# Optimization experiments

Measured on AMD Instinct MI355X. Metric: run time of the kernel, lower is better.

The kernel has to match this reference:

```python
import jax, jax.numpy as jnp
import numpy as np

B, N, D_IN = 8, 8192, 13
RATIO, R, K = 0.25, 0.2, 32


def setup_inputs() -> dict:
    key = jax.random.key(0)
    k1, k2, k3, k4 = jax.random.split(key, 4)
    x = jax.random.normal(k1, (B, N, D_IN), dtype=jnp.float32)
    pos = jax.random.uniform(k2, (B, N, 3), dtype=jnp.float32)
    batch = jnp.broadcast_to(jnp.arange(B, dtype=jnp.int32)[:, None], (B, N))
    W1 = jax.random.normal(k3, (D_IN + 3, 64), dtype=jnp.float32) * 0.1
    b1 = jnp.zeros((64,), jnp.float32)
    W2 = jax.random.normal(k4, (64, 128), dtype=jnp.float32) * 0.1
    b2 = jnp.zeros((128,), jnp.float32)
    return {"x": x, "pos": pos, "batch": batch, "W1": W1, "b1": b1, "W2": W2, "b2": b2}


def _fps_single(p, M):
    """Deterministic farthest point sampling (start at index 0). p: [N,3] -> [M] int32."""
    n = p.shape[0]

    def step(carry, _):
        mind, last = carry
        d = jnp.sum((p - p[last]) ** 2, axis=-1)
        mind = jnp.minimum(mind, d)
        nxt = jnp.argmax(mind).astype(jnp.int32)
        return (mind, nxt), nxt

    init = (jnp.full((n,), 1e10, p.dtype), jnp.int32(0))
    _, rest = jax.lax.scan(step, init, None, length=M - 1)
    return jnp.concatenate([jnp.zeros((1,), jnp.int32), rest])


def reference(x, pos, batch, W1, b1, W2, b2):
    M = int(RATIO * N)
    # --- FPS per cloud ---
    idx = jax.vmap(lambda p: _fps_single(p, M))(pos)              # [B, M]
    pos_s = jnp.take_along_axis(pos, idx[..., None], axis=1)      # [B, M, 3]
    # --- radius ball query: first K in-ball neighbors by point index ---
    d2 = jnp.sum((pos_s[:, :, None, :] - pos[:, None, :, :]) ** 2, axis=-1)  # [B, M, N]
    within = d2 <= R * R
    rank = jnp.where(within, jnp.arange(N, dtype=jnp.int32), N)   # invalid -> N
    negv, nbr = jax.lax.top_k(-rank, K)                           # K smallest ranks
    valid = negv > -N                                             # [B, M, K]
    # --- gather -> local_nn MLP -> masked max-scatter (PointNetConv) ---
    x_j = jax.vmap(lambda a, i: a[i])(x, nbr)                     # [B, M, K, D_IN]
    pos_j = jax.vmap(lambda a, i: a[i])(pos, nbr)                 # [B, M, K, 3]
    feat = jnp.concatenate([x_j, pos_j - pos_s[:, :, None, :]], axis=-1)
    h = jax.nn.relu(feat @ W1 + b1)
    h = jax.nn.relu(h @ W2 + b2)                                  # [B, M, K, 128]
    h = jnp.where(valid[..., None], h, -jnp.inf)
    x_out = jnp.max(h, axis=2)                                    # [B, M, 128]
    batch_s = jnp.take_along_axis(batch, idx, axis=1)             # [B, M]
    return x_out, pos_s, batch_s
```

## Files before the change

kernel.cpp:

```cpp
#include <hip/hip_runtime.h>
#include <cstddef>

#define B_   8
#define N_   8192
#define M_   2048
#define K_   32
#define DIN_ 13

typedef _Float16 f16x8 __attribute__((ext_vector_type(8)));
typedef float    f32x4 __attribute__((ext_vector_type(4)));

template <int CTRL>
__device__ __forceinline__ float dppmax(float v) {
  int o = __builtin_amdgcn_update_dpp(
      (int)0xff800000, __float_as_int(v), CTRL, 0xF, 0xF, false);
  return fmaxf(v, __int_as_float(o));
}
template <int CTRL>
__device__ __forceinline__ float dppminf(float v) {
  int o = __builtin_amdgcn_update_dpp(
      (int)0x7f800000, __float_as_int(v), CTRL, 0xF, 0xF, false);
  return fminf(v, __int_as_float(o));
}
template <int CTRL>
__device__ __forceinline__ unsigned dppminu(unsigned v) {
  unsigned o = (unsigned)__builtin_amdgcn_update_dpp(
      (int)0xFFFFFFFF, (int)v, CTRL, 0xF, 0xF, false);
  return v < o ? v : o;
}
__device__ __forceinline__ float wave_reduce_max(float v) {
  v = dppmax<0x111>(v); v = dppmax<0x112>(v); v = dppmax<0x114>(v);
  v = dppmax<0x118>(v); v = dppmax<0x142>(v); v = dppmax<0x143>(v);
  return __int_as_float(__builtin_amdgcn_readlane(__float_as_int(v), 63));
}
__device__ __forceinline__ unsigned wave_reduce_min_u32(unsigned v) {
  v = dppminu<0x111>(v); v = dppminu<0x112>(v); v = dppminu<0x114>(v);
  v = dppminu<0x118>(v); v = dppminu<0x142>(v); v = dppminu<0x143>(v);
  return (unsigned)__builtin_amdgcn_readlane((int)v, 63);
}

__global__ __launch_bounds__(1024, 4) void fps_kernel(
    const float* __restrict__ pos,
    float* __restrict__ pos_s,
    float* __restrict__ batch_s)
{
  const int b    = blockIdx.x;
  const int t    = threadIdx.x;
  const int lane = t & 63;
  const int wid  = t >> 6;
  const float* p = pos + (size_t)b * N_ * 3;

  __shared__ float px_l[N_], py_l[N_], pz_l[N_];
  __shared__ int   r2o[N_];
  __shared__ int   vbase[512];
  __shared__ int   vcur[512];
  __shared__ int   wsum[8];
  __shared__ unsigned long long kslot[3];

  for (int mm = t; mm < M_; mm += 1024)
    batch_s[b * M_ + mm] = (float)b;
  if (t < 512) vcur[t] = 0;
  if (t == 0) { kslot[0] = 0ull; kslot[1] = 0ull; kslot[2] = 0ull; }
  __syncthreads();

  int vid[8];
#pragma unroll
  for (int i = 0; i < 8; ++i) {
    int j = t + 1024 * i;
    float x = p[j * 3 + 0], y = p[j * 3 + 1], z = p[j * 3 + 2];
    px_l[j] = x; py_l[j] = y; pz_l[j] = z;
    int ix = (int)(x * 8.f); ix = ix < 0 ? 0 : (ix > 7 ? 7 : ix);
    int iy = (int)(y * 8.f); iy = iy < 0 ? 0 : (iy > 7 ? 7 : iy);
    int iz = (int)(z * 8.f); iz = iz < 0 ? 0 : (iz > 7 ? 7 : iz);
    int v = (ix & 1) | ((iy & 1) << 1) | ((iz & 1) << 2) |
            (((ix >> 1) & 1) << 3) | (((iy >> 1) & 1) << 4) |
            (((iz >> 1) & 1) << 5) |
            ((ix >> 2) << 6) | ((iy >> 2) << 7) | ((iz >> 2) << 8);
    vid[i] = v;
    atomicAdd(&vcur[v], 1);
  }
  __syncthreads();

  int h = 0, sc = 0;
  if (t < 512) {
    h = vcur[t]; sc = h;
#pragma unroll
    for (int d = 1; d < 64; d <<= 1) {
      int o = __shfl_up(sc, d);
      if (lane >= d) sc += o;
    }
    if (lane == 63) wsum[wid] = sc;
  }
  __syncthreads();
  if (t < 8) {
    int v = wsum[t]; int inc = v;
#pragma unroll
    for (int d = 1; d < 8; d <<= 1) {
      int o = __shfl_up(inc, d);
      if (t >= d) inc += o;
    }
    wsum[t] = inc - v;
  }
  __syncthreads();
  if (t < 512) { vbase[t] = sc - h + wsum[t >> 6]; vcur[t] = 0; }
  __syncthreads();

#pragma unroll
  for (int i = 0; i < 8; ++i) {
    int j = t + 1024 * i;
    int r = vbase[vid[i]] + atomicAdd(&vcur[vid[i]], 1);
    r2o[r] = j;
  }
  __syncthreads();

  float px[8], py[8], pz[8], mind[8]; int oi[8];
#pragma unroll
  for (int i = 0; i < 8; ++i) {
    int o = r2o[t * 8 + i];
    oi[i] = o;
    px[i] = px_l[o]; py[i] = py_l[o]; pz[i] = pz_l[o];
    mind[i] = 1e10f;
  }
#pragma unroll
  for (int i = 0; i < 8; ++i) {
    asm volatile("" : "+v"(px[i]), "+v"(py[i]), "+v"(pz[i]));
  }

  float bxmin = px[0], bxmax = px[0], bymin = py[0], bymax = py[0],
        bzmin = pz[0], bzmax = pz[0];
#pragma unroll
  for (int i = 1; i < 8; ++i) {
    bxmin = fminf(bxmin, px[i]); bxmax = fmaxf(bxmax, px[i]);
    bymin = fminf(bymin, py[i]); bymax = fmaxf(bymax, py[i]);
    bzmin = fminf(bzmin, pz[i]); bzmax = fmaxf(bzmax, pz[i]);
  }

  float lx = px_l[0], ly = py_l[0], lz = pz_l[0];
  if (t == 0) {
    pos_s[(size_t)b * M_ * 3 + 0] = lx;
    pos_s[(size_t)b * M_ * 3 + 1] = ly;
    pos_s[(size_t)b * M_ * 3 + 2] = lz;
  }

  float ltm = 1e10f;
  float cwm = 0.f;
  unsigned cmin = 0xFFFFFFFFu;
  int sl = 1;
  int rs = 0;

  for (int s = 1; s < M_; ++s) {
    float cx = fmaxf(fmaxf(bxmin - lx, lx - bxmax), 0.f);
    float cy = fmaxf(fmaxf(bymin - ly, ly - bymax), 0.f);
    float cz = fmaxf(fmaxf(bzmin - lz, lz - bzmax), 0.f);
    float LB = (cx * cx + cy * cy) + cz * cz;
    bool lp = (LB * 0.999999f < ltm);
    if (__ballot(lp) != 0ull) {
      float tmax;
      {
#pragma clang fp contract(off)
#pragma unroll
        for (int i = 0; i < 8; ++i) {
          float dx = px[i] - lx, dy = py[i] - ly, dz = pz[i] - lz;
          float d  = (dx * dx + dy * dy) + dz * dz;
          mind[i]  = fminf(mind[i], d);
        }
        float m0 = fmaxf(mind[0], mind[1]), m1 = fmaxf(mind[2], mind[3]);
        float m2 = fmaxf(mind[4], mind[5]), m3 = fmaxf(mind[6], mind[7]);
        tmax = fmaxf(fmaxf(m0, m1), fmaxf(m2, m3));
      }
      ltm = tmax;
      const float wm = wave_reduce_max(tmax);
      cwm = wm;
      unsigned cc = 0xFFFFFFFFu;
#pragma unroll
      for (int i = 0; i < 8; ++i) {
        unsigned cand = (mind[i] == wm) ? (unsigned)oi[i] : 0xFFFFFFFFu;
        cc = cc < cand ? cc : cand;
      }
      cmin = wave_reduce_min_u32(cc);
    }
    if (lane == 0) {
      unsigned long long key =
          ((unsigned long long)__float_as_uint(cwm) << 32) |
          (unsigned long long)(0xFFFFFFFFu - cmin);
      atomicMax(&kslot[sl], key);
    }
    __syncthreads();
    if (t == 0) kslot[rs] = 0ull;
    const unsigned long long kk = kslot[sl];
    const int wj  = (int)(0xFFFFFFFFu - (unsigned int)(kk & 0xFFFFFFFFull));
    const int wju = (int)__builtin_amdgcn_readfirstlane(wj);
    lx = px_l[wju]; ly = py_l[wju]; lz = pz_l[wju];
    if (t == 0) {
      size_t o2 = ((size_t)b * M_ + s) * 3;
      pos_s[o2 + 0] = lx; pos_s[o2 + 1] = ly; pos_s[o2 + 2] = lz;
    }
    sl = (sl == 2) ? 0 : sl + 1;
    rs = (rs == 2) ? 0 : rs + 1;
  }
}

__global__ __launch_bounds__(256) void prep_kernel(
    const float* __restrict__ W1, const float* __restrict__ W2,
    _Float16* __restrict__ w1t, _Float16* __restrict__ w2t)
{
  int t = blockIdx.x * 256 + threadIdx.x;
  if (t < 8192) {
    int n = t >> 6, k = t & 63;
    w2t[t] = (_Float16)W2[k * 128 + n];
  }
  int u = t - 8192;
  if (u >= 0 && u < 1024) {
    int n = u >> 4, k = u & 15;
    w1t[u] = (_Float16)W1[k * 64 + n];
  }
}

__global__ __launch_bounds__(64) void sa_kernel(
    const float* __restrict__ x,
    const float* __restrict__ pos,
    const float* __restrict__ b1,
    const float* __restrict__ b2,
    const float* __restrict__ pos_s,
    const _Float16* __restrict__ w1t,
    const _Float16* __restrict__ w2t,
    float* __restrict__ x_out)
{
  const int blk  = blockIdx.x;
  const int b    = blk >> 11;
  const int m    = blk & 2047;
  const int lane = threadIdx.x;
  const int l15  = lane & 15;
  const int quad = lane >> 4;

  __shared__ int      nbr[K_];
  __shared__ _Float16 featb[K_][24];
  __shared__ _Float16 h1b[K_][72];

  const float* pb = pos + (size_t)b * N_ * 3;
  const float* xb = x   + (size_t)b * N_ * DIN_;
  const size_t so = ((size_t)b * M_ + m) * 3;
  const float sx = pos_s[so + 0];
  const float sy = pos_s[so + 1];
  const float sz = pos_s[so + 2];
  const float R2 = (float)(0.2 * 0.2);

  int cnt = 0;
  for (int base = 0; base < N_ && cnt < K_; base += 64) {
    int j = base + lane;
    float qx = pb[j * 3 + 0], qy = pb[j * 3 + 1], qz = pb[j * 3 + 2];
    bool win;
    {
#pragma clang fp contract(off)
      float dx = sx - qx, dy = sy - qy, dz = sz - qz;
      float d2 = (dx * dx + dy * dy) + dz * dz;
      win = d2 <= R2;
    }
    unsigned long long mk = __ballot(win);
    int rank = (int)__popcll(mk & ((1ull << lane) - 1ull));
    if (win) {
      int slot = cnt + rank;
      if (slot < K_) nbr[slot] = j;
    }
    cnt += (int)__popcll(mk);
  }
  const int valid = cnt < K_ ? cnt : K_;
  __syncthreads();

  for (int tq = lane; tq < K_ * 16; tq += 64) {
    int r = tq >> 4, i = tq & 15;
    float v = 0.f;
    if (r < valid) {
      int j = nbr[r];
      if (i < DIN_) {
        v = xb[j * DIN_ + i];
      } else {
        float c = (i == 13) ? sx : (i == 14) ? sy : sz;
        float q = pb[j * 3 + (i - 13)];
        v = q - c;
      }
    }
    featb[r][i] = (_Float16)v;
  }
  __syncthreads();

  f16x8 fz;
#pragma unroll
  for (int i = 0; i < 8; ++i) fz[i] = (_Float16)0;

  f16x8 a1[2], b1f[4];
#pragma unroll
  for (int mt = 0; mt < 2; ++mt)
    a1[mt] = (quad < 2) ? *(const f16x8*)&featb[mt * 16 + l15][quad * 8] : fz;
#pragma unroll
  for (int nt = 0; nt < 4; ++nt)
    b1f[nt] = (quad < 2) ? *(const f16x8*)&w1t[(nt * 16 + l15) * 16 + quad * 8]
                         : fz;

#pragma unroll
  for (int mt = 0; mt < 2; ++mt) {
#pragma unroll
    for (int nt = 0; nt < 4; ++nt) {
      f32x4 c = {0.f, 0.f, 0.f, 0.f};
      c = __builtin_amdgcn_mfma_f32_16x16x32_f16(a1[mt], b1f[nt], c, 0, 0, 0);
      float bb = b1[nt * 16 + l15];
#pragma unroll
      for (int r = 0; r < 4; ++r) {
        float v = c[r] + bb;
        h1b[mt * 16 + quad * 4 + r][nt * 16 + l15] =
            (_Float16)(v > 0.f ? v : 0.f);
      }
    }
  }
  __syncthreads();

  f16x8 a2[2][2];
#pragma unroll
  for (int mt = 0; mt < 2; ++mt)
#pragma unroll
    for (int kt = 0; kt < 2; ++kt)
      a2[mt][kt] = *(const f16x8*)&h1b[mt * 16 + l15][kt * 32 + quad * 8];

  float* o = x_out + ((size_t)b * M_ + m) * 128;
#pragma unroll
  for (int nt = 0; nt < 8; ++nt) {
    f16x8 b20 = *(const f16x8*)&w2t[(nt * 16 + l15) * 64 + 0 * 32 + quad * 8];
    f16x8 b21 = *(const f16x8*)&w2t[(nt * 16 + l15) * 64 + 1 * 32 + quad * 8];
    f32x4 c0 = {0.f, 0.f, 0.f, 0.f}, c1 = {0.f, 0.f, 0.f, 0.f};
    c0 = __builtin_amdgcn_mfma_f32_16x16x32_f16(a2[0][0], b20, c0, 0, 0, 0);
    c0 = __builtin_amdgcn_mfma_f32_16x16x32_f16(a2[0][1], b21, c0, 0, 0, 0);
    c1 = __builtin_amdgcn_mfma_f32_16x16x32_f16(a2[1][0], b20, c1, 0, 0, 0);
    c1 = __builtin_amdgcn_mfma_f32_16x16x32_f16(a2[1][1], b21, c1, 0, 0, 0);
    float bv = b2[nt * 16 + l15];
    float acc = -INFINITY;
#pragma unroll
    for (int r = 0; r < 4; ++r) {
      int row0 = quad * 4 + r;
      int row1 = 16 + quad * 4 + r;
      float v0 = c0[r] + bv; v0 = v0 > 0.f ? v0 : 0.f;
      float v1 = c1[r] + bv; v1 = v1 > 0.f ? v1 : 0.f;
      if (row0 < valid) acc = fmaxf(acc, v0);
      if (row1 < valid) acc = fmaxf(acc, v1);
    }
    acc = fmaxf(acc, __shfl_xor(acc, 16));
    acc = fmaxf(acc, __shfl_xor(acc, 32));
    if (quad == 0) o[nt * 16 + l15] = acc;
  }
}

extern "C" void kernel_launch(void* const* d_in, const int* in_sizes, int n_in,
                              void* d_out, int out_size, void* d_ws, size_t ws_size,
                              hipStream_t stream) {
  (void)in_sizes; (void)n_in; (void)ws_size; (void)out_size;
  const float* x   = (const float*)d_in[0];
  const float* pos = (const float*)d_in[1];
  const float* W1  = (const float*)d_in[3];
  const float* b1  = (const float*)d_in[4];
  const float* W2  = (const float*)d_in[5];
  const float* b2  = (const float*)d_in[6];

  float* out     = (float*)d_out;
  float* x_out   = out;
  float* pos_s   = out + (size_t)B_ * M_ * 128;
  float* batch_s = pos_s + (size_t)B_ * M_ * 3;

  _Float16* w1t = (_Float16*)d_ws;
  _Float16* w2t = w1t + 1024;

  prep_kernel<<<36, 256, 0, stream>>>(W1, W2, w1t, w2t);
  fps_kernel<<<B_, 1024, 0, stream>>>(pos, pos_s, batch_s);
  sa_kernel<<<B_ * M_, 64, 0, stream>>>(x, pos, b1, b2, pos_s, w1t, w2t, x_out);
}
```

Baseline: 1.503 ms.

## Halve FPS block size and replace shared atomicMax with per-wave key DPP reduction

The farthest-point-sampling kernel now runs 512 threads per cloud, each holding 16 points instead of 8. Each step, every wave writes its packed (distance, index) key to a double-buffered shared slot instead of doing a shared 64-bit atomicMax. After the barrier, each wave reduces the 8 wave keys with a DPP max and reads the winner, which removes the triple-slot rotation and its reset. The aim is a cheaper per-step barrier and no atomic contention on the sequential critical path, at the cost of more distance work per thread and more register pressure.

```diff
diff --git a/kernel.cpp b/kernel.cpp
--- a/kernel.cpp
+++ b/kernel.cpp
@@ -17,12 +17,6 @@
   return fmaxf(v, __int_as_float(o));
 }
 template <int CTRL>
-__device__ __forceinline__ float dppminf(float v) {
-  int o = __builtin_amdgcn_update_dpp(
-      (int)0x7f800000, __float_as_int(v), CTRL, 0xF, 0xF, false);
-  return fminf(v, __int_as_float(o));
-}
-template <int CTRL>
 __device__ __forceinline__ unsigned dppminu(unsigned v) {
   unsigned o = (unsigned)__builtin_amdgcn_update_dpp(
       (int)0xFFFFFFFF, (int)v, CTRL, 0xF, 0xF, false);
@@ -38,8 +32,18 @@
   v = dppminu<0x118>(v); v = dppminu<0x142>(v); v = dppminu<0x143>(v);
   return (unsigned)__builtin_amdgcn_readlane((int)v, 63);
 }
-
-__global__ __launch_bounds__(1024, 4) void fps_kernel(
+template <int CTRL>
+__device__ __forceinline__ void dppmax_u64(unsigned &hi, unsigned &lo) {
+  unsigned ohi = (unsigned)__builtin_amdgcn_update_dpp(
+      0, (int)hi, CTRL, 0xF, 0xF, false);
+  unsigned olo = (unsigned)__builtin_amdgcn_update_dpp(
+      0, (int)lo, CTRL, 0xF, 0xF, false);
+  bool g = (ohi > hi) || (ohi == hi && olo > lo);
+  hi = g ? ohi : hi;
+  lo = g ? olo : lo;
+}
+
+__global__ __launch_bounds__(512) void fps_kernel(
     const float* __restrict__ pos,
     float* __restrict__ pos_s,
     float* __restrict__ batch_s)
@@ -55,18 +59,17 @@
   __shared__ int   vbase[512];
   __shared__ int   vcur[512];
   __shared__ int   wsum[8];
-  __shared__ unsigned long long kslot[3];
-
-  for (int mm = t; mm < M_; mm += 1024)
+  __shared__ unsigned long long wkey[2][8];
+
+  for (int mm = t; mm < M_; mm += 512)
     batch_s[b * M_ + mm] = (float)b;
-  if (t < 512) vcur[t] = 0;
-  if (t == 0) { kslot[0] = 0ull; kslot[1] = 0ull; kslot[2] = 0ull; }
-  __syncthreads();
-
-  int vid[8];
-#pragma unroll
-  for (int i = 0; i < 8; ++i) {
-    int j = t + 1024 * i;
+  vcur[t] = 0;
+  __syncthreads();
+
+  int vid[16];
+#pragma unroll
+  for (int i = 0; i < 16; ++i) {
+    int j = t + 512 * i;
     float x = p[j * 3 + 0], y = p[j * 3 + 1], z = p[j * 3 + 2];
     px_l[j] = x; py_l[j] = y; pz_l[j] = z;
     int ix = (int)(x * 8.f); ix = ix < 0 ? 0 : (ix > 7 ? 7 : ix);
@@ -81,16 +84,13 @@
   }
   __syncthreads();
 
-  int h = 0, sc = 0;
-  if (t < 512) {
-    h = vcur[t]; sc = h;
-#pragma unroll
-    for (int d = 1; d < 64; d <<= 1) {
-      int o = __shfl_up(sc, d);
-      if (lane >= d) sc += o;
-    }
-    if (lane == 63) wsum[wid] = sc;
-  }
+  int h = vcur[t], sc = h;
+#pragma unroll
+  for (int d = 1; d < 64; d <<= 1) {
+    int o = __shfl_up(sc, d);
+    if (lane >= d) sc += o;
+  }
+  if (lane == 63) wsum[wid] = sc;
   __syncthreads();
   if (t < 8) {
     int v = wsum[t]; int inc = v;
@@ -102,34 +102,35 @@
     wsum[t] = inc - v;
   }
   __syncthreads();
-  if (t < 512) { vbase[t] = sc - h + wsum[t >> 6]; vcur[t] = 0; }
-  __syncthreads();
-
-#pragma unroll
-  for (int i = 0; i < 8; ++i) {
-    int j = t + 1024 * i;
+  vbase[t] = sc - h + wsum[t >> 6];
+  vcur[t]  = 0;
+  __syncthreads();
+
+#pragma unroll
+  for (int i = 0; i < 16; ++i) {
+    int j = t + 512 * i;
     int r = vbase[vid[i]] + atomicAdd(&vcur[vid[i]], 1);
     r2o[r] = j;
   }
   __syncthreads();
 
-  float px[8], py[8], pz[8], mind[8]; int oi[8];
-#pragma unroll
-  for (int i = 0; i < 8; ++i) {
-    int o = r2o[t * 8 + i];
+  float px[16], py[16], pz[16], mind[16]; int oi[16];
+#pragma unroll
+  for (int i = 0; i < 16; ++i) {
+    int o = r2o[t * 16 + i];
     oi[i] = o;
     px[i] = px_l[o]; py[i] = py_l[o]; pz[i] = pz_l[o];
     mind[i] = 1e10f;
   }
 #pragma unroll
-  for (int i = 0; i < 8; ++i) {
+  for (int i = 0; i < 16; ++i) {
     asm volatile("" : "+v"(px[i]), "+v"(py[i]), "+v"(pz[i]));
   }
 
   float bxmin = px[0], bxmax = px[0], bymin = py[0], bymax = py[0],
         bzmin = pz[0], bzmax = pz[0];
 #pragma unroll
-  for (int i = 1; i < 8; ++i) {
+  for (int i = 1; i < 16; ++i) {
     bxmin = fminf(bxmin, px[i]); bxmax = fmaxf(bxmax, px[i]);
     bymin = fminf(bymin, py[i]); bymax = fmaxf(bymax, py[i]);
     bzmin = fminf(bzmin, pz[i]); bzmax = fmaxf(bzmax, pz[i]);
@@ -143,10 +144,7 @@
   }
 
   float ltm = 1e10f;
-  float cwm = 0.f;
-  unsigned cmin = 0xFFFFFFFFu;
-  int sl = 1;
-  int rs = 0;
+  unsigned long long ckey = 0;
 
   for (int s = 1; s < M_; ++s) {
     float cx = fmaxf(fmaxf(bxmin - lx, lx - bxmax), 0.f);
@@ -159,44 +157,43 @@
       {
 #pragma clang fp contract(off)
 #pragma unroll
-        for (int i = 0; i < 8; ++i) {
+        for (int i = 0; i < 16; ++i) {
           float dx = px[i] - lx, dy = py[i] - ly, dz = pz[i] - lz;
           float d  = (dx * dx + dy * dy) + dz * dz;
           mind[i]  = fminf(mind[i], d);
         }
-        float m0 = fmaxf(mind[0], mind[1]), m1 = fmaxf(mind[2], mind[3]);
-        float m2 = fmaxf(mind[4], mind[5]), m3 = fmaxf(mind[6], mind[7]);
+        float m0 = fmaxf(fmaxf(mind[0],  mind[1]),  fmaxf(mind[2],  mind[3]));
+        float m1 = fmaxf(fmaxf(mind[4],  mind[5]),  fmaxf(mind[6],  mind[7]));
+        float m2 = fmaxf(fmaxf(mind[8],  mind[9]),  fmaxf(mind[10], mind[11]));
+        float m3 = fmaxf(fmaxf(mind[12], mind[13]), fmaxf(mind[14], mind[15]));
         tmax = fmaxf(fmaxf(m0, m1), fmaxf(m2, m3));
       }
       ltm = tmax;
       const float wm = wave_reduce_max(tmax);
-      cwm = wm;
       unsigned cc = 0xFFFFFFFFu;
 #pragma unroll
-      for (int i = 0; i < 8; ++i) {
+      for (int i = 0; i < 16; ++i) {
         unsigned cand = (mind[i] == wm) ? (unsigned)oi[i] : 0xFFFFFFFFu;
         cc = cc < cand ? cc : cand;
       }
-      cmin = wave_reduce_min_u32(cc);
-    }
-    if (lane == 0) {
-      unsigned long long key =
-          ((unsigned long long)__float_as_uint(cwm) << 32) |
-          (unsigned long long)(0xFFFFFFFFu - cmin);
-      atomicMax(&kslot[sl], key);
-    }
+      unsigned cmin = wave_reduce_min_u32(cc);
+      ckey = ((unsigned long long)__float_as_uint(wm) << 32) |
+             (unsigned long long)(0xFFFFFFFFu - cmin);
+    }
+    if (lane == 0) wkey[s & 1][wid] = ckey;
     __syncthreads();
-    if (t == 0) kslot[rs] = 0ull;
-    const unsigned long long kk = kslot[sl];
-    const int wj  = (int)(0xFFFFFFFFu - (unsigned int)(kk & 0xFFFFFFFFull));
-    const int wju = (int)__builtin_amdgcn_readfirstlane(wj);
+    unsigned long long kk = wkey[s & 1][lane & 7];
+    unsigned khi = (unsigned)(kk >> 32), klo = (unsigned)kk;
+    dppmax_u64<0x111>(khi, klo);
+    dppmax_u64<0x112>(khi, klo);
+    dppmax_u64<0x114>(khi, klo);
+    const unsigned wlo = (unsigned)__builtin_amdgcn_readlane((int)klo, 63);
+    const int wju = (int)(0xFFFFFFFFu - wlo);
     lx = px_l[wju]; ly = py_l[wju]; lz = pz_l[wju];
     if (t == 0) {
       size_t o2 = ((size_t)b * M_ + s) * 3;
       pos_s[o2 + 0] = lx; pos_s[o2 + 1] = ly; pos_s[o2 + 2] = lz;
     }
-    sl = (sl == 2) ? 0 : sl + 1;
-    rs = (rs == 2) ? 0 : rs + 1;
   }
 }
 
@@ -368,6 +365,6 @@
   _Float16* w2t = w1t + 1024;
 
   prep_kernel<<<36, 256, 0, stream>>>(W1, W2, w1t, w2t);
-  fps_kernel<<<B_, 1024, 0, stream>>>(pos, pos_s, batch_s);
+  fps_kernel<<<B_, 512, 0, stream>>>(pos, pos_s, batch_s);
   sa_kernel<<<B_ * M_, 64, 0, stream>>>(x, pos, b1, b2, pos_s, w1t, w2t, x_out);
 }
```

After: 1.793 ms. +19.3%, slower.
